# Kernel optimization log

Measured on AMD Instinct MI355X. Metric: run time of the kernel, lower is better.

The kernel has to match this reference:

```python
import jax, jax.numpy as jnp
import numpy as np

# Correlation2D hyperparameters (FlowNet-style cost volume, corr_multiply=1)
PAD = 3          # pad_size
K = 3            # kernel_size (odd)
MD = 1           # max_displacement
S1 = 1           # stride1 (output stride)
S2 = 1           # stride2 (displacement stride)
KR = (K - 1) // 2            # kernel radius
GR = MD // S2                # neighborhood grid radius
D = 2 * GR + 1               # displacements per axis -> D*D output channels


def setup_inputs() -> dict:
    key = jax.random.key(0)
    k1, k2 = jax.random.split(key)
    B, C, H, W = 4, 96, 256, 256
    input1 = jax.random.normal(k1, (B, C, H, W), dtype=jnp.float32)
    input2 = jax.random.normal(k2, (B, C, H, W), dtype=jnp.float32)
    return {"input1": input1, "input2": input2}


def _correlation(x1, x2):
    B, C, H, W = x1.shape
    p1 = jnp.pad(x1, ((0, 0), (0, 0), (PAD, PAD), (PAD, PAD)))
    p2 = jnp.pad(x2, ((0, 0), (0, 0), (PAD, PAD), (PAD, PAD)))
    Hp, Wp = H + 2 * PAD, W + 2 * PAD
    # patch centers y1 = y*S1 + MD + KR; output size per FlowNet corr_cuda
    Ho = (Hp - 2 * KR - 2 * MD - 1) // S1 + 1
    Wo = (Wp - 2 * KR - 2 * MD - 1) // S1 + 1
    # extra pad so shifted slices of p2 are always in-bounds (zeros never read)
    p2e = jnp.pad(p2, ((0, 0), (0, 0), (MD, MD), (MD, MD)))
    box = jnp.ones((1, 1, K, K), x1.dtype)
    norm = jnp.asarray(K * K * C, x1.dtype)
    outs = []
    for tj in range(-GR, GR + 1):       # channel order: (tj+GR)*D + (ti+GR)
        for ti in range(-GR, GR + 1):
            dy, dx = tj * S2, ti * S2
            shifted = p2e[:, :, MD + dy:MD + dy + Hp, MD + dx:MD + dx + Wp]
            # channel-summed pointwise product: (B,1,Hp,Wp)
            q = jnp.sum(p1 * shifted, axis=1, keepdims=True)
            # K x K box window sum (VALID): index o = top-left = y1-KR
            s = jax.lax.conv_general_dilated(q, box, (1, 1), 'VALID')
            # window top-left for output y is y*S1 + MD
            s = s[:, 0, MD:MD + (Ho - 1) * S1 + 1:S1, MD:MD + (Wo - 1) * S1 + 1:S1]
            outs.append(s)
    return jnp.stack(outs, axis=1) / norm   # (B, D*D, Ho, Wo)


def reference(input1, input2):
    return _correlation(input1, input2)
```

## Files before the change

kernel.cpp:

```cpp
#include <hip/hip_runtime.h>

#define HC 256
#define WC 256
#define CC 96
#define BB 4
#define OH 258
#define OW 258
#define PLANE 65536
#define NPAIR 128
#define CGW 24
#define K2_JOBS (BB * 9 * OH)
#define K2_BLOCKS ((K2_JOBS + 3) / 4)
#define WS_NEEDED ((size_t)BB * 9 * PLANE * 4)

__device__ __forceinline__ float4 ld4(const float* p){ return *reinterpret_cast<const float4*>(p); }
__device__ __forceinline__ void st4(float* p, float4 v){ *reinterpret_cast<float4*>(p) = v; }

__device__ __forceinline__ void tap6(float4& A, float4& B, float4& C, const float4 a,
                                     float w0, float w1, float w2, float w3, float w4, float w5)
{
    A.x = fmaf(a.x, w0, A.x); A.y = fmaf(a.y, w1, A.y); A.z = fmaf(a.z, w2, A.z); A.w = fmaf(a.w, w3, A.w);
    B.x = fmaf(a.x, w1, B.x); B.y = fmaf(a.y, w2, B.y); B.z = fmaf(a.z, w3, B.z); B.w = fmaf(a.w, w4, B.w);
    C.x = fmaf(a.x, w2, C.x); C.y = fmaf(a.y, w3, C.y); C.z = fmaf(a.z, w4, C.z); C.w = fmaf(a.w, w5, C.w);
}

__global__ __launch_bounds__(256) void corr_r_kernel(
    const float* __restrict__ x1, const float* __restrict__ x2, float* __restrict__ rws)
{
    const int tid = threadIdx.x;
    const int g   = tid >> 6;
    const int t   = tid & 63;
    const int bid  = blockIdx.x;
    const int pair = (bid & 7) * (NPAIR / 8) + (bid >> 3);
    const int b    = blockIdx.y;
    const int h0 = 2 * pair, h1 = h0 + 1;
    const int wq = 4 * t;

    const bool vm1 = (h0 > 0);
    const bool vp2 = (h1 < HC - 1);
    const int rm1 = vm1 ? h0 - 1 : 0;
    const int rp2 = vp2 ? h1 + 1 : HC - 1;

    const float* p1b = x1 + (size_t)(b * CC + g * CGW) * PLANE;
    const float* p2b = x2 + (size_t)(b * CC + g * CGW) * PLANE;

    const int o1a = h0 * WC + wq, o1b = h1 * WC + wq;
    const int o20 = rm1 * WC + wq, o21 = h0 * WC + wq, o22 = h1 * WC + wq, o23 = rp2 * WC + wq;

    const float4 fz = make_float4(0.f, 0.f, 0.f, 0.f);
    float4 acc0[9], acc1[9];
#pragma unroll
    for (int d = 0; d < 9; ++d) { acc0[d] = fz; acc1[d] = fz; }

    float4 A0[2], A1[2], Q0[2], Q1[2], Q2[2], Q3[2];

#define ISSUE(s, cc)                                                           \
    do {                                                                       \
        const float* P1 = p1b + (size_t)(cc) * PLANE;                          \
        const float* P2 = p2b + (size_t)(cc) * PLANE;                          \
        A0[s] = ld4(P1 + o1a);                                                 \
        A1[s] = ld4(P1 + o1b);                                                 \
        Q0[s] = vm1 ? ld4(P2 + o20) : fz;                                      \
        Q1[s] = ld4(P2 + o21);                                                 \
        Q2[s] = ld4(P2 + o22);                                                 \
        Q3[s] = vp2 ? ld4(P2 + o23) : fz;                                      \
    } while (0)

#define COMPUTE_STEP(s)                                                                          \
    do {                                                                                         \
        float pw0 = __shfl_up(Q0[s].w, 1), nx0 = __shfl_down(Q0[s].x, 1);                        \
        float pw1 = __shfl_up(Q1[s].w, 1), nx1 = __shfl_down(Q1[s].x, 1);                        \
        float pw2 = __shfl_up(Q2[s].w, 1), nx2 = __shfl_down(Q2[s].x, 1);                        \
        float pw3 = __shfl_up(Q3[s].w, 1), nx3 = __shfl_down(Q3[s].x, 1);                        \
        if (t == 0)  { pw0 = 0; pw1 = 0; pw2 = 0; pw3 = 0; }                                     \
        if (t == 63) { nx0 = 0; nx1 = 0; nx2 = 0; nx3 = 0; }                                     \
        tap6(acc0[0], acc0[1], acc0[2], A0[s], pw0, Q0[s].x, Q0[s].y, Q0[s].z, Q0[s].w, nx0);    \
        tap6(acc0[3], acc0[4], acc0[5], A0[s], pw1, Q1[s].x, Q1[s].y, Q1[s].z, Q1[s].w, nx1);    \
        tap6(acc1[0], acc1[1], acc1[2], A1[s], pw1, Q1[s].x, Q1[s].y, Q1[s].z, Q1[s].w, nx1);    \
        tap6(acc0[6], acc0[7], acc0[8], A0[s], pw2, Q2[s].x, Q2[s].y, Q2[s].z, Q2[s].w, nx2);    \
        tap6(acc1[3], acc1[4], acc1[5], A1[s], pw2, Q2[s].x, Q2[s].y, Q2[s].z, Q2[s].w, nx2);    \
        tap6(acc1[6], acc1[7], acc1[8], A1[s], pw3, Q3[s].x, Q3[s].y, Q3[s].z, Q3[s].w, nx3);    \
    } while (0)

    ISSUE(0, 0);
    ISSUE(1, 1);
#pragma unroll 2
    for (int c = 0; c < CGW; ++c) {
        const int s = c & 1;
        COMPUTE_STEP(s);
        if (c + 2 < CGW) ISSUE(s, c + 2);
    }
#undef ISSUE
#undef COMPUTE_STEP

    __shared__ __align__(16) float red[9][2][WC];
    for (int r = 0; r < 4; ++r) {
        if (g == r) {
#pragma unroll
            for (int d = 0; d < 9; ++d) {
                float* d0p = &red[d][0][wq];
                float* d1p = &red[d][1][wq];
                if (r == 0) { st4(d0p, acc0[d]); st4(d1p, acc1[d]); }
                else {
                    float4 v0 = ld4(d0p), v1 = ld4(d1p);
                    v0.x += acc0[d].x; v0.y += acc0[d].y; v0.z += acc0[d].z; v0.w += acc0[d].w;
                    v1.x += acc1[d].x; v1.y += acc1[d].y; v1.z += acc1[d].z; v1.w += acc1[d].w;
                    st4(d0p, v0); st4(d1p, v1);
                }
            }
        }
        __syncthreads();
    }

    for (int idx = tid; idx < 9 * 2 * 64; idx += 256) {
        const int t2 = idx & 63;
        const int ds = idx >> 6;
        const int s  = ds & 1;
        const int d  = ds >> 1;
        float4 v = ld4(&red[d][s][4 * t2]);
        st4(rws + (((size_t)(b * 9 + d) * HC) + (h0 + s)) * WC + 4 * t2, v);
    }
}

__global__ __launch_bounds__(256) void corr_box_kernel(
    const float* __restrict__ rws, float* __restrict__ out)
{
    const int tid = threadIdx.x;
    const int wid = tid >> 6, t = tid & 63;
    const int job = blockIdx.x * 4 + wid;
    if (job >= K2_JOBS) return;
    const int y  = job % OH;
    const int bd = job / OH;
    const float* rp = rws + (size_t)bd * PLANE;

    float4 s4 = make_float4(0.f, 0.f, 0.f, 0.f);
    float s256 = 0.f, s257 = 0.f;
#pragma unroll
    for (int k = 0; k < 3; ++k) {
        const int rr = y - 2 + k;
        if ((unsigned)rr < (unsigned)HC) {
            float4 q = ld4(rp + rr * WC + 4 * t);
            float pz = __shfl_up(q.z, 1);
            float pw = __shfl_up(q.w, 1);
            if (t == 0) { pz = 0.f; pw = 0.f; }
            s4.x += pz + pw + q.x;
            s4.y += pw + q.x + q.y;
            s4.z += q.x + q.y + q.z;
            s4.w += q.y + q.z + q.w;
            s256 += q.z + q.w;
            s257 += q.w;
        }
    }
    float* orow = out + ((size_t)bd * OH + y) * OW;
    const float sc = 1.0f / 864.0f;
    orow[4 * t]     = s4.x * sc;
    orow[4 * t + 1] = s4.y * sc;
    orow[4 * t + 2] = s4.z * sc;
    orow[4 * t + 3] = s4.w * sc;
    if (t == 63) { orow[256] = s256 * sc; orow[257] = s257 * sc; }
}

#define FBTOX 30
#define FBTOY 14
__global__ __launch_bounds__(256) void corr2d_fb(
    const float* __restrict__ x1, const float* __restrict__ x2, float* __restrict__ out)
{
    const int tx = threadIdx.x, ty = threadIdx.y;
    const int bx = blockIdx.x, by = blockIdx.y, b = blockIdx.z;
    const int x0 = bx * FBTOX, y0 = by * FBTOY;
    const int w = x0 - 2 + tx;
    const int h0 = y0 - 2 + ty, h1 = h0 + 8;
    const size_t plane = (size_t)HC * WC;
    const float* p1 = x1 + (size_t)b * CC * plane;
    const float* p2 = x2 + (size_t)b * CC * plane;
    float acc[2][9];
#pragma unroll
    for (int i = 0; i < 2; ++i)
#pragma unroll
        for (int d = 0; d < 9; ++d) acc[i][d] = 0.f;
    const bool interior = (x0 >= 3) && (x0 + 30 <= WC - 1) && (y0 >= 3) && (y0 + 14 <= HC - 1);
    if (interior) {
        const float* q1 = p1 + (size_t)(h0 * WC + w);
        const float* q2 = p2 + (size_t)(h0 * WC + w);
        for (int c = 0; c < CC; ++c) {
            const float a0 = q1[0];
            const float a1 = q1[8 * WC];
#pragma unroll
            for (int tj = -1; tj <= 1; ++tj)
#pragma unroll
                for (int ti = -1; ti <= 1; ++ti) {
                    const int d = (tj + 1) * 3 + (ti + 1);
                    acc[0][d] = fmaf(a0, q2[tj * WC + ti], acc[0][d]);
                    acc[1][d] = fmaf(a1, q2[(tj + 8) * WC + ti], acc[1][d]);
                }
            q1 += plane; q2 += plane;
        }
    } else {
        int rows[6]; bool rv[6];
        const int hh[6] = {h0 - 1, h0, h0 + 1, h1 - 1, h1, h1 + 1};
#pragma unroll
        for (int j = 0; j < 6; ++j) {
            rv[j] = ((unsigned)hh[j] < (unsigned)HC);
            int hcl = hh[j] < 0 ? 0 : (hh[j] > HC - 1 ? HC - 1 : hh[j]);
            rows[j] = hcl * WC;
        }
        int cols[3]; bool cv[3];
#pragma unroll
        for (int i = 0; i < 3; ++i) {
            int ww = w - 1 + i;
            cv[i] = ((unsigned)ww < (unsigned)WC);
            cols[i] = ww < 0 ? 0 : (ww > WC - 1 ? WC - 1 : ww);
        }
        const bool v0 = ((unsigned)h0 < (unsigned)HC) && ((unsigned)w < (unsigned)WC);
        const bool v1 = ((unsigned)h1 < (unsigned)HC) && ((unsigned)w < (unsigned)WC);
        const int wcl = w < 0 ? 0 : (w > WC - 1 ? WC - 1 : w);
        const int off1_0 = (h0 < 0 ? 0 : (h0 > HC - 1 ? HC - 1 : h0)) * WC + wcl;
        const int off1_1 = (h1 < 0 ? 0 : (h1 > HC - 1 ? HC - 1 : h1)) * WC + wcl;
        const float* q1 = p1;
        const float* q2 = p2;
        for (int c = 0; c < CC; ++c) {
            const float a0 = v0 ? q1[off1_0] : 0.f;
            const float a1 = v1 ? q1[off1_1] : 0.f;
#pragma unroll
            for (int jr = 0; jr < 3; ++jr)
#pragma unroll
                for (int i = 0; i < 3; ++i) {
                    const int d = jr * 3 + i;
                    const float u0 = (rv[jr] && cv[i])     ? q2[rows[jr] + cols[i]]     : 0.f;
                    const float u1 = (rv[jr + 3] && cv[i]) ? q2[rows[jr + 3] + cols[i]] : 0.f;
                    acc[0][d] = fmaf(a0, u0, acc[0][d]);
                    acc[1][d] = fmaf(a1, u1, acc[1][d]);
                }
            q1 += plane; q2 += plane;
        }
    }
    __shared__ float rl[9][16][32];
#pragma unroll
    for (int d = 0; d < 9; ++d) {
        rl[d][ty][tx]     = acc[0][d];
        rl[d][ty + 8][tx] = acc[1][d];
    }
    __syncthreads();
    const int tid = ty * 32 + tx;
    for (int j = tid; j < FBTOX * FBTOY; j += 256) {
        const int oy = j / FBTOX, ox = j - oy * FBTOX;
        const int y = y0 + oy, x = x0 + ox;
        if (y < OH && x < OW) {
#pragma unroll
            for (int d = 0; d < 9; ++d) {
                float s = 0.f;
#pragma unroll
                for (int a = 0; a < 3; ++a)
#pragma unroll
                    for (int b2 = 0; b2 < 3; ++b2)
                        s += rl[d][oy + a][ox + b2];
                out[(((size_t)b * 9 + d) * OH + y) * OW + x] = s * (1.0f / 864.0f);
            }
        }
    }
}

extern "C" void kernel_launch(void* const* d_in, const int* in_sizes, int n_in,
                              void* d_out, int out_size, void* d_ws, size_t ws_size,
                              hipStream_t stream) {
    const float* x1 = (const float*)d_in[0];
    const float* x2 = (const float*)d_in[1];
    float* out = (float*)d_out;
    if (ws_size >= WS_NEEDED) {
        float* rws = (float*)d_ws;
        hipLaunchKernelGGL(corr_r_kernel, dim3(NPAIR, BB), dim3(256), 0, stream, x1, x2, rws);
        hipLaunchKernelGGL(corr_box_kernel, dim3(K2_BLOCKS), dim3(256), 0, stream, rws, out);
    } else {
        hipLaunchKernelGGL(corr2d_fb,
                           dim3((OW + FBTOX - 1) / FBTOX, (OH + FBTOY - 1) / FBTOY, BB),
                           dim3(32, 8), 0, stream, x1, x2, out);
    }
}
```

Measured before the change: 43.10 us.

## Split channel reduction across eight waves with tree reduction in LDS

```diff
diff --git a/kernel.cpp b/kernel.cpp
--- a/kernel.cpp
+++ b/kernel.cpp
@@ -8,7 +8,8 @@
 #define OW 258
 #define PLANE 65536
 #define NPAIR 128
-#define CGW 24
+#define NW 8
+#define CGW 12
 #define K2_JOBS (BB * 9 * OH)
 #define K2_BLOCKS ((K2_JOBS + 3) / 4)
 #define WS_NEEDED ((size_t)BB * 9 * PLANE * 4)
@@ -24,7 +25,7 @@
     C.x = fmaf(a.x, w2, C.x); C.y = fmaf(a.y, w3, C.y); C.z = fmaf(a.z, w4, C.z); C.w = fmaf(a.w, w5, C.w);
 }
 
-__global__ __launch_bounds__(256) void corr_r_kernel(
+__global__ __launch_bounds__(512) void corr_r_kernel(
     const float* __restrict__ x1, const float* __restrict__ x2, float* __restrict__ rws)
 {
     const int tid = threadIdx.x;
@@ -93,33 +94,61 @@
 #undef ISSUE
 #undef COMPUTE_STEP
 
-    __shared__ __align__(16) float red[9][2][WC];
-    for (int r = 0; r < 4; ++r) {
-        if (g == r) {
-#pragma unroll
-            for (int d = 0; d < 9; ++d) {
-                float* d0p = &red[d][0][wq];
-                float* d1p = &red[d][1][wq];
-                if (r == 0) { st4(d0p, acc0[d]); st4(d1p, acc1[d]); }
-                else {
-                    float4 v0 = ld4(d0p), v1 = ld4(d1p);
-                    v0.x += acc0[d].x; v0.y += acc0[d].y; v0.z += acc0[d].z; v0.w += acc0[d].w;
-                    v1.x += acc1[d].x; v1.y += acc1[d].y; v1.z += acc1[d].z; v1.w += acc1[d].w;
-                    st4(d0p, v0); st4(d1p, v1);
-                }
-            }
-        }
-        __syncthreads();
-    }
-
-    for (int idx = tid; idx < 9 * 2 * 64; idx += 256) {
-        const int t2 = idx & 63;
-        const int ds = idx >> 6;
-        const int s  = ds & 1;
-        const int d  = ds >> 1;
-        float4 v = ld4(&red[d][s][4 * t2]);
-        st4(rws + (((size_t)(b * 9 + d) * HC) + (h0 + s)) * WC + 4 * t2, v);
-    }
+    __shared__ __align__(16) float buf[2][9][2][WC];
+
+#define WBUF(i)                                                              \
+    do {                                                                     \
+        _Pragma("unroll")                                                    \
+        for (int d = 0; d < 9; ++d) {                                        \
+            st4(&buf[i][d][0][wq], acc0[d]);                                 \
+            st4(&buf[i][d][1][wq], acc1[d]);                                 \
+        }                                                                    \
+    } while (0)
+#define ABUF(i)                                                              \
+    do {                                                                     \
+        _Pragma("unroll")                                                    \
+        for (int d = 0; d < 9; ++d) {                                        \
+            float4 v0 = ld4(&buf[i][d][0][wq]);                              \
+            float4 v1 = ld4(&buf[i][d][1][wq]);                              \
+            acc0[d].x += v0.x; acc0[d].y += v0.y;                            \
+            acc0[d].z += v0.z; acc0[d].w += v0.w;                            \
+            acc1[d].x += v1.x; acc1[d].y += v1.y;                            \
+            acc1[d].z += v1.z; acc1[d].w += v1.w;                            \
+        }                                                                    \
+    } while (0)
+
+    if (g == 1) WBUF(0);
+    if (g == 5) WBUF(1);
+    __syncthreads();
+    if (g == 0) ABUF(0);
+    if (g == 4) ABUF(1);
+    __syncthreads();
+    if (g == 3) WBUF(0);
+    if (g == 7) WBUF(1);
+    __syncthreads();
+    if (g == 2) ABUF(0);
+    if (g == 6) ABUF(1);
+    __syncthreads();
+    if (g == 2) WBUF(0);
+    if (g == 6) WBUF(1);
+    __syncthreads();
+    if (g == 0) ABUF(0);
+    if (g == 4) ABUF(1);
+    __syncthreads();
+    if (g == 4) WBUF(0);
+    __syncthreads();
+
+    if (g == 0) {
+        ABUF(0);
+#pragma unroll
+        for (int d = 0; d < 9; ++d) {
+            float* base = rws + (((size_t)(b * 9 + d) * HC) + h0) * WC;
+            st4(base + wq, acc0[d]);
+            st4(base + WC + wq, acc1[d]);
+        }
+    }
+#undef WBUF
+#undef ABUF
 }
 
 __global__ __launch_bounds__(256) void corr_box_kernel(
@@ -268,7 +297,7 @@
     float* out = (float*)d_out;
     if (ws_size >= WS_NEEDED) {
         float* rws = (float*)d_ws;
-        hipLaunchKernelGGL(corr_r_kernel, dim3(NPAIR, BB), dim3(256), 0, stream, x1, x2, rws);
+        hipLaunchKernelGGL(corr_r_kernel, dim3(NPAIR, BB), dim3(512), 0, stream, x1, x2, rws);
         hipLaunchKernelGGL(corr_box_kernel, dim3(K2_BLOCKS), dim3(256), 0, stream, rws, out);
     } else {
         hipLaunchKernelGGL(corr2d_fb,
```

Measured after the change: 47.78 us. 1.11x slower.
